# Kernel tuning notes

Measured on AMD Instinct MI355X. Metric: run time of the kernel, lower is better.

The kernel has to match this reference:

```python
import jax, jax.numpy as jnp
import numpy as np

B, T, C = 2, 2048, 1024
H, HS = 16, 64          # num_heads, head_size; H*HS == C
FF = 4 * C
EPS = 1e-5


def setup_inputs() -> dict:
    key = jax.random.key(0)
    ks = jax.random.split(key, 10)
    s = 0.02
    return {
        "x": jax.random.normal(ks[0], (B, T, C), dtype=jnp.float32),
        "Wq": jax.random.normal(ks[1], (H, C, HS), dtype=jnp.float32) * s,
        "Wk": jax.random.normal(ks[2], (H, C, HS), dtype=jnp.float32) * s,
        "Wv": jax.random.normal(ks[3], (H, C, HS), dtype=jnp.float32) * s,
        "p": jnp.ones((H,), dtype=jnp.float32),  # per-head learnable scale, init 1
        "Wproj": jax.random.normal(ks[4], (C, C), dtype=jnp.float32) * s,
        "W1": jax.random.normal(ks[5], (C, FF), dtype=jnp.float32) * s,
        "W2": jax.random.normal(ks[6], (FF, C), dtype=jnp.float32) * s,
        "ln1_w": jnp.ones((C,), dtype=jnp.float32),
        "ln1_b": jnp.zeros((C,), dtype=jnp.float32),
        "ln2_w": jnp.ones((C,), dtype=jnp.float32),
        "ln2_b": jnp.zeros((C,), dtype=jnp.float32),
    }


def _layernorm(x, w, b):
    mu = jnp.mean(x, axis=-1, keepdims=True)
    var = jnp.mean(jnp.square(x - mu), axis=-1, keepdims=True)
    return (x - mu) * jax.lax.rsqrt(var + EPS) * w + b


def reference(x, Wq, Wk, Wv, p, Wproj, W1, W2, ln1_w, ln1_b, ln2_w, ln2_b):
    # --- multi-head causal self-attention (dropout p=0 -> identity) ---
    h = _layernorm(x, ln1_w, ln1_b)
    q = jnp.einsum("btc,hcs->bhts", h, Wq)  # [B,H,T,HS]
    k = jnp.einsum("btc,hcs->bhts", h, Wk)
    v = jnp.einsum("btc,hcs->bhts", h, Wv)
    scale = p ** (-0.5)  # per-head scale, p init to 1
    wei = jnp.einsum("bhts,bhks->bhtk", q, k) * scale[None, :, None, None]
    causal = jnp.tril(jnp.ones((T, T), dtype=bool))
    wei = jnp.where(causal[None, None], wei, -jnp.inf)
    wei = jax.nn.softmax(wei, axis=-1)
    att = jnp.einsum("bhtk,bhks->bhts", wei, v)          # [B,H,T,HS]
    att = att.transpose(0, 2, 1, 3).reshape(B, T, C)     # concat heads
    sa = att @ Wproj
    x = x + sa
    # --- feed-forward (activation_id=0 -> ReLU) ---
    h2 = _layernorm(x, ln2_w, ln2_b)
    ff = jax.nn.relu(h2 @ W1) @ W2
    return x + ff
```

## Files before the change

### kernel.cpp

```cpp
#include <hip/hip_runtime.h>


typedef _Float16 f16;
typedef _Float16 f16x8 __attribute__((ext_vector_type(8)));
typedef _Float16 f16x4v __attribute__((ext_vector_type(4)));
typedef float f32x4 __attribute__((ext_vector_type(4)));

static constexpr int Tn = 2048;
static constexpr int Cn = 1024;
static constexpr int HSn = 64;

__device__ __forceinline__ void glds16(const f16* g, f16* l) {
    __builtin_amdgcn_global_load_lds((const __attribute__((address_space(1))) void*)g,
                                     (__attribute__((address_space(3))) void*)l,
                                     16, 0, 0);
}

#define VMCNT(N) asm volatile("s_waitcnt vmcnt(" #N ")" ::: "memory")
__device__ __forceinline__ void barrier_raw() {
    asm volatile("" ::: "memory");
    __builtin_amdgcn_s_barrier();
    asm volatile("" ::: "memory");
}

__device__ __forceinline__ unsigned cvt_pk_u32(float a, float b) {
    auto v = __builtin_amdgcn_cvt_pkrtz(a, b);
    union { __fp16 h2 __attribute__((ext_vector_type(2))); unsigned u; } c;
    c.h2 = v;
    return c.u;
}

__global__ __launch_bounds__(256) void ln_kernel(const float* __restrict__ x,
                                                 const float* __restrict__ w,
                                                 const float* __restrict__ b,
                                                 f16* __restrict__ out) {
    int row = blockIdx.x;
    const float* xr = x + (size_t)row * Cn;
    int tid = threadIdx.x, l = tid & 63, wv = tid >> 6;
    float4 v = *(const float4*)(xr + tid * 4);
    float s = v.x + v.y + v.z + v.w;
    float sq = v.x * v.x + v.y * v.y + v.z * v.z + v.w * v.w;
#pragma unroll
    for (int off = 32; off > 0; off >>= 1) {
        s += __shfl_down(s, off);
        sq += __shfl_down(sq, off);
    }
    __shared__ float red[8];
    if (l == 0) { red[wv] = s; red[wv + 4] = sq; }
    __syncthreads();
    float ts = red[0] + red[1] + red[2] + red[3];
    float tq = red[4] + red[5] + red[6] + red[7];
    float mean = ts * (1.0f / Cn);
    float var = tq * (1.0f / Cn) - mean * mean;
    float rstd = rsqrtf(var + 1e-5f);
    float4 wv4 = *(const float4*)(w + tid * 4);
    float4 bv4 = *(const float4*)(b + tid * 4);
    f16x4v o;
    o[0] = (f16)((v.x - mean) * rstd * wv4.x + bv4.x);
    o[1] = (f16)((v.y - mean) * rstd * wv4.y + bv4.y);
    o[2] = (f16)((v.z - mean) * rstd * wv4.z + bv4.z);
    o[3] = (f16)((v.w - mean) * rstd * wv4.w + bv4.w);
    *(f16x4v*)(out + (size_t)row * Cn + tid * 4) = o;
}

__global__ __launch_bounds__(256) void tr_cast_f32(const float* __restrict__ in, int irs,
                                                   f16* __restrict__ out, int ors) {
    __shared__ float tile[32][33];
    int r0 = blockIdx.x * 32, c0 = blockIdx.y * 32;
    int t = threadIdx.x;
    int rr = t >> 3, c4 = (t & 7) * 4;
    float4 v = *(const float4*)(in + (size_t)(r0 + rr) * irs + c0 + c4);
    tile[rr][c4] = v.x; tile[rr][c4 + 1] = v.y; tile[rr][c4 + 2] = v.z; tile[rr][c4 + 3] = v.w;
    __syncthreads();
    int cc = t >> 3, r4 = (t & 7) * 4;
    f16x4v o;
    o[0] = (f16)tile[r4][cc];
    o[1] = (f16)tile[r4 + 1][cc];
    o[2] = (f16)tile[r4 + 2][cc];
    o[3] = (f16)tile[r4 + 3][cc];
    *(f16x4v*)(out + (size_t)(c0 + cc) * ors + r0 + r4) = o;
}

__global__ __launch_bounds__(256) void tr_cast_qkv(const float* __restrict__ Wq,
                                                   const float* __restrict__ Wk,
                                                   const float* __restrict__ Wv,
                                                   f16* __restrict__ out) {
    int z = blockIdx.z;
    int qkv = z >> 4, h = z & 15;
    const float* in = (qkv == 0 ? Wq : qkv == 1 ? Wk : Wv) + (size_t)h * Cn * HSn;
    f16* o = out + (size_t)(qkv * Cn + h * HSn) * Cn;
    __shared__ float tile[32][33];
    int r0 = blockIdx.x * 32, c0 = blockIdx.y * 32;
    int t = threadIdx.x;
    int rr = t >> 3, c4 = (t & 7) * 4;
    float4 v = *(const float4*)(in + (size_t)(r0 + rr) * HSn + c0 + c4);
    tile[rr][c4] = v.x; tile[rr][c4 + 1] = v.y; tile[rr][c4 + 2] = v.z; tile[rr][c4 + 3] = v.w;
    __syncthreads();
    int cc = t >> 3, r4 = (t & 7) * 4;
    f16x4v ov;
    ov[0] = (f16)tile[r4][cc];
    ov[1] = (f16)tile[r4 + 1][cc];
    ov[2] = (f16)tile[r4 + 2][cc];
    ov[3] = (f16)tile[r4 + 3][cc];
    *(f16x4v*)(o + (size_t)(c0 + cc) * Cn + r0 + r4) = ov;
}

__global__ __launch_bounds__(256) void tr_vT(const f16* __restrict__ QKV, f16* __restrict__ vT) {
    int bh = blockIdx.z;
    int b = bh >> 4, h = bh & 15;
    const f16* in = QKV + (size_t)b * Tn * 3072 + 2048 + h * HSn;
    f16* out = vT + (size_t)bh * HSn * Tn;
    int r0 = blockIdx.x * 64;
    __shared__ __align__(16) f16 tile[64][72];
    int t = threadIdx.x;
#pragma unroll
    for (int i = 0; i < 2; i++) {
        int f = i * 256 + t;
        int rr = f >> 3, c8 = (f & 7) * 8;
        *(uint4*)(&tile[rr][c8]) = *(const uint4*)(in + (size_t)(r0 + rr) * 3072 + c8);
    }
    __syncthreads();
#pragma unroll
    for (int i = 0; i < 2; i++) {
        int f = i * 256 + t;
        int cc = f >> 3, r8 = (f & 7) * 8;
        union { f16 h[8]; uint4 v; } u;
#pragma unroll
        for (int j = 0; j < 8; j++) u.h[j] = tile[r8 + j][cc];
        *(uint4*)(out + (size_t)cc * Tn + r0 + r8) = u.v;
    }
}

template <int EPI>
__global__ __launch_bounds__(512, 2) void gemm8(const f16* __restrict__ A, const f16* __restrict__ Bt,
                                                f16* __restrict__ Cout, int M, int N, int K) {
    __shared__ __align__(16) f16 Abuf[4][8192];
    __shared__ __align__(16) f16 Bbuf[4][8192];
    int wg = blockIdx.x;
    int xcd = wg & 7, idx = wg >> 3;
    int bm = xcd * 2 + (idx & 1), bn = idx >> 1;
    int tid = threadIdx.x, l = tid & 63, w = tid >> 6;
    int wr = w >> 2, wc = w & 3;

    f32x4 acc[8][4];
#pragma unroll
    for (int m = 0; m < 8; m++)
#pragma unroll
        for (int n = 0; n < 4; n++) acc[m][n] = f32x4{0.f, 0.f, 0.f, 0.f};

    int l15 = l & 15;
    int lane_off = l15 * 32 + (((l >> 4) ^ ((l15 >> 1) & 3)) << 3);
    const f16* Afr = &Abuf[0][wr * 4096 + lane_off];
    const f16* Bfr = &Bbuf[0][(wc >> 1) * 4096 + (wc & 1) * 2048 + lane_off];

    int srow = w * 16 + (l >> 2);
    int schunk = (l & 3) ^ ((l >> 3) & 3);
    const f16* agp = A + (size_t)(bm * 256 + srow) * K + schunk * 8;
    const f16* bgp = Bt + (size_t)(bn * 256 + srow) * K + schunk * 8;
    const size_t rK = (size_t)128 * K;
    f16* dstA = &Abuf[0][w * 512];
    f16* dstB = &Bbuf[0][w * 512];

    auto stage = [&](int kt, int bf) {
        int k0 = kt * 32;
        glds16(agp + k0, dstA + bf * 8192);
        glds16(agp + rK + k0, dstA + bf * 8192 + 4096);
        glds16(bgp + k0, dstB + bf * 8192);
        glds16(bgp + rK + k0, dstB + bf * 8192 + 4096);
    };

    int NT = K >> 5;
    stage(0, 0);
    stage(1, 1);
    stage(2, 2);
    for (int t = 0; t < NT; ++t) {
        int cb = t & 3;
        if (t < NT - 2) VMCNT(8);
        else if (t == NT - 2) VMCNT(4);
        else VMCNT(0);
        barrier_raw();
        const f16* Ab = Afr + cb * 8192;
        const f16* Bb = Bfr + cb * 8192;
        f16x8 af[4], bf4[4];
#pragma unroll
        for (int m = 0; m < 4; m++) af[m] = *(const f16x8*)(Ab + m * 512);
#pragma unroll
        for (int n = 0; n < 4; n++) bf4[n] = *(const f16x8*)(Bb + n * 512);
        if (t + 3 < NT) stage(t + 3, (t + 3) & 3);
        __builtin_amdgcn_s_setprio(1);
#pragma unroll
        for (int m = 0; m < 4; m++)
#pragma unroll
            for (int n = 0; n < 4; n++)
                acc[m][n] = __builtin_amdgcn_mfma_f32_16x16x32_f16(af[m], bf4[n], acc[m][n], 0, 0, 0);
        __builtin_amdgcn_s_setprio(0);
        barrier_raw();
#pragma unroll
        for (int m = 0; m < 4; m++) af[m] = *(const f16x8*)(Ab + (m + 4) * 512);
        __builtin_amdgcn_s_setprio(1);
#pragma unroll
        for (int m = 0; m < 4; m++)
#pragma unroll
            for (int n = 0; n < 4; n++)
                acc[m + 4][n] = __builtin_amdgcn_mfma_f32_16x16x32_f16(af[m], bf4[n], acc[m + 4][n], 0, 0, 0);
        __builtin_amdgcn_s_setprio(0);
    }

    int row0 = bm * 256 + wr * 128 + (l >> 4) * 4;
    int col0 = bn * 256 + wc * 64 + (l & 15);
#pragma unroll
    for (int m = 0; m < 8; m++) {
#pragma unroll
        for (int n = 0; n < 4; n++) {
#pragma unroll
            for (int r = 0; r < 4; r++) {
                size_t idx = (size_t)(row0 + m * 16 + r) * N + (col0 + n * 16);
                float v = acc[m][n][r];
                if constexpr (EPI == 1) v = fmaxf(v, 0.f);
                Cout[idx] = (f16)v;
            }
        }
    }
}

__device__ __forceinline__ void l2_map(int& bm, int& bn) {
    int wg = blockIdx.y * 32 + blockIdx.x;
    int x = wg & 7, idx = wg >> 3;
    bm = x * 4 + (idx & 3);
    bn = idx >> 2;
}

template <int EPI>
__global__ __launch_bounds__(512) void gemm_ks(const f16* __restrict__ A, const f16* __restrict__ Bt,
                                               void* __restrict__ Cout, const float* __restrict__ resid,
                                               int M, int N, int K) {
    __shared__ __align__(16) char smem[131072];
    f16* As = (f16*)smem;
    f16* Bs = (f16*)(smem + 65536);
    int bm, bn;
    l2_map(bm, bn);
    int tid = threadIdx.x, l = tid & 63, w = tid >> 6;
    int grp = w >> 2, wl = w & 3;
    int wr = wl >> 1, wc = wl & 1;
    int Kh = K >> 1;
    int KT = Kh >> 5;

    f32x4 acc[4][4];
#pragma unroll
    for (int m = 0; m < 4; m++)
#pragma unroll
        for (int n = 0; n < 4; n++) acc[m][n] = f32x4{0.f, 0.f, 0.f, 0.f};

    int schunk = (l & 3) ^ ((l >> 3) & 3);
    const f16* agp = A + (size_t)(bm * 128 + wl * 16 + (l >> 2)) * K + grp * Kh + schunk * 8;
    const f16* bgp = Bt + (size_t)(bn * 128 + wl * 16 + (l >> 2)) * K + grp * Kh + schunk * 8;
    const size_t half = (size_t)64 * K;
    f16* Ab = As + grp * 16384;
    f16* Bb = Bs + grp * 16384;

    auto stage = [&](int kt, int bf) {
        size_t k0 = (size_t)kt * 32;
        glds16(agp + k0, Ab + bf * 4096 + wl * 512);
        glds16(agp + half + k0, Ab + bf * 4096 + 2048 + wl * 512);
        glds16(bgp + k0, Bb + bf * 4096 + wl * 512);
        glds16(bgp + half + k0, Bb + bf * 4096 + 2048 + wl * 512);
    };

    int l15 = l & 15;
    int rbase = (wr * 64 + l15) * 32 + (((l >> 4) ^ ((l15 >> 1) & 3)) << 3);
    int cbase = (wc * 64 + l15) * 32 + (((l >> 4) ^ ((l15 >> 1) & 3)) << 3);

    stage(0, 0);
    stage(1, 1);
    stage(2, 2);
    for (int kt = 0; kt < KT; ++kt) {
        int cb = kt & 3;
        if (kt < KT - 2) VMCNT(8);
        else if (kt == KT - 2) VMCNT(4);
        else VMCNT(0);
        barrier_raw();
        if (kt + 3 < KT) stage(kt + 3, (kt + 3) & 3);
        f16x8 af[4], bfr[4];
#pragma unroll
        for (int m = 0; m < 4; m++) af[m] = *(const f16x8*)(Ab + cb * 4096 + rbase + m * 512);
#pragma unroll
        for (int n = 0; n < 4; n++) bfr[n] = *(const f16x8*)(Bb + cb * 4096 + cbase + n * 512);
        __builtin_amdgcn_s_setprio(1);
#pragma unroll
        for (int m = 0; m < 4; m++)
#pragma unroll
            for (int n = 0; n < 4; n++)
                acc[m][n] = __builtin_amdgcn_mfma_f32_16x16x32_f16(af[m], bfr[n], acc[m][n], 0, 0, 0);
        __builtin_amdgcn_s_setprio(0);
    }
    __syncthreads();

    float* red = (float*)smem;
#pragma unroll
    for (int m = 0; m < 4; m++) {
        if (grp == 1) {
#pragma unroll
            for (int n = 0; n < 4; n++)
                *(f32x4*)(red + wl * 1280 + l * 20 + n * 4) = acc[m][n];
        }
        __syncthreads();
        if (grp == 0) {
#pragma unroll
            for (int n = 0; n < 4; n++)
                acc[m][n] += *(const f32x4*)(red + wl * 1280 + l * 20 + n * 4);
        }
        __syncthreads();
    }

    if (grp == 0) {
        int row0 = bm * 128 + wr * 64 + (l >> 4) * 4;
        int col0 = bn * 128 + wc * 64 + (l & 15);
#pragma unroll
        for (int m = 0; m < 4; m++) {
#pragma unroll
            for (int n = 0; n < 4; n++) {
#pragma unroll
                for (int r = 0; r < 4; r++) {
                    size_t idx = (size_t)(row0 + m * 16 + r) * N + (col0 + n * 16);
                    float v = acc[m][n][r];
                    if constexpr (EPI == 0) ((f16*)Cout)[idx] = (f16)v;
                    else if constexpr (EPI == 1) ((f16*)Cout)[idx] = (f16)fmaxf(v, 0.f);
                    else ((float*)Cout)[idx] = v + resid[idx];
                }
            }
        }
    }
}

__global__ __launch_bounds__(256) void attn_kernel(const f16* __restrict__ QKV,
                                                   const f16* __restrict__ vT,
                                                   const float* __restrict__ p,
                                                   f16* __restrict__ att) {
    int i = blockIdx.x;
    int bh = (i & 7) * 4 + ((i >> 3) & 3);
    int qt = 31 - (i >> 5);
    int b = bh >> 4, h = bh & 15;
    int tid = threadIdx.x, w = tid >> 6, l = tid & 63;
    float sc2 = rsqrtf(p[h]) * 1.44269504f;

    __shared__ __align__(16) f16 Ks[2][4096];
    __shared__ __align__(16) f16 Vs[2][4096];
    __shared__ __align__(16) f16 Ps[4][16 * 80];
    f16* Pw = &Ps[w][0];

    int srow0 = tid >> 3;
    int c0 = (tid & 7) ^ (srow0 & 7);
    const f16* Kg = QKV + (size_t)b * Tn * 3072 + 1024 + h * HSn;
    const f16* Vg = vT + (size_t)bh * HSn * Tn;
    const f16* Kg0 = Kg + (size_t)srow0 * 3072 + c0 * 8;
    const f16* Kg1 = Kg + (size_t)(srow0 + 32) * 3072 + c0 * 8;
    const f16* Vg0 = Vg + (size_t)srow0 * Tn + c0 * 8;
    const f16* Vg1 = Vg + (size_t)(srow0 + 32) * Tn + c0 * 8;
    int dl = w * 512 + l * 8;

    int foff[8];
#pragma unroll
    for (int n = 0; n < 4; n++)
#pragma unroll
        for (int ks = 0; ks < 2; ks++)
            foff[n * 2 + ks] = (n * 16 + (l & 15)) * 128 +
                               (((ks * 32 + (l >> 4) * 8) * 2) ^ ((l & 7) << 4));

    int qg = qt * 64 + w * 16 + (l & 15);
    int qo = qt * 64 + w * 16 + (l >> 4) * 4;
    const f16* qptr = QKV + (size_t)(b * Tn + qg) * 3072 + h * HSn + (l >> 4) * 8;
    f16x8 qf0 = *(const f16x8*)(qptr);
    f16x8 qf1 = *(const f16x8*)(qptr + 32);
    f16 sch = (f16)sc2;
#pragma unroll
    for (int j = 0; j < 8; j++) { qf0[j] *= sch; qf1[j] *= sch; }

    f32x4 o[4];
#pragma unroll
    for (int nf = 0; nf < 4; nf++) o[nf] = f32x4{0.f, 0.f, 0.f, 0.f};
    float m_r = -1e30f, l_r = 0.f;

    int nt = qt + 1;
    uint4 kr0 = *(const uint4*)(Kg0);
    uint4 kr1 = *(const uint4*)(Kg1);
    uint4 vr0 = *(const uint4*)(Vg0);
    uint4 vr1 = *(const uint4*)(Vg1);
    *(uint4*)(&Ks[0][dl]) = kr0;
    *(uint4*)(&Ks[0][2048 + dl]) = kr1;
    *(uint4*)(&Vs[0][dl]) = vr0;
    *(uint4*)(&Vs[0][2048 + dl]) = vr1;
    __syncthreads();
    for (int t = 0; t < nt; ++t) {
        int kv0 = t * 64;
        if (t + 1 < nt) {
            size_t ko = (size_t)(kv0 + 64) * 3072;
            kr0 = *(const uint4*)(Kg0 + ko);
            kr1 = *(const uint4*)(Kg1 + ko);
            vr0 = *(const uint4*)(Vg0 + kv0 + 64);
            vr1 = *(const uint4*)(Vg1 + kv0 + 64);
        }
        const char* Kb = (const char*)&Ks[t & 1][0];
        const char* Vb = (const char*)&Vs[t & 1][0];
        f32x4 s[4];
#pragma unroll
        for (int n = 0; n < 4; n++) s[n] = f32x4{0.f, 0.f, 0.f, 0.f};
        __builtin_amdgcn_s_setprio(1);
#pragma unroll
        for (int n = 0; n < 4; n++)
#pragma unroll
            for (int ks = 0; ks < 2; ks++) {
                f16x8 kf = *(const f16x8*)(Kb + foff[n * 2 + ks]);
                s[n] = __builtin_amdgcn_mfma_f32_16x16x32_f16(kf, ks == 0 ? qf0 : qf1, s[n], 0, 0, 0);
            }
        __builtin_amdgcn_s_setprio(0);
        if (t == qt) {
            int rel = qg - kv0;
#pragma unroll
            for (int n = 0; n < 4; n++)
#pragma unroll
                for (int r = 0; r < 4; r++) {
                    int kvr = n * 16 + (l >> 4) * 4 + r;
                    if (kvr > rel) s[n][r] = -1e30f;
                }
        }
        float tmax = -1e30f;
#pragma unroll
        for (int n = 0; n < 4; n++)
#pragma unroll
            for (int r = 0; r < 4; r++) tmax = fmaxf(tmax, s[n][r]);
        float lmul = 1.f;
        if (__any(tmax > m_r + 8.f)) {
            float rmax = fmaxf(tmax, __shfl_xor(tmax, 16));
            rmax = fmaxf(rmax, __shfl_xor(rmax, 32));
            float mnew = fmaxf(m_r, rmax);
            lmul = exp2f(m_r - mnew);
            m_r = mnew;
            float ar[4];
#pragma unroll
            for (int r = 0; r < 4; r++) ar[r] = __shfl(lmul, (l >> 4) * 4 + r);
#pragma unroll
            for (int nf = 0; nf < 4; nf++)
#pragma unroll
                for (int r = 0; r < 4; r++) o[nf][r] *= ar[r];
        }
        float rsum = 0.f;
#pragma unroll
        for (int n = 0; n < 4; n++) {
            float e0 = exp2f(s[n][0] - m_r), e1 = exp2f(s[n][1] - m_r);
            float e2 = exp2f(s[n][2] - m_r), e3 = exp2f(s[n][3] - m_r);
            rsum += (e0 + e1) + (e2 + e3);
            union { unsigned u[2]; f16x4v h4; } u;
            u.u[0] = cvt_pk_u32(e0, e1);
            u.u[1] = cvt_pk_u32(e2, e3);
            *(f16x4v*)(&Pw[(l & 15) * 80 + n * 16 + (l >> 4) * 4]) = u.h4;
        }
        l_r = l_r * lmul + rsum;
        f16x8 pa0 = *(const f16x8*)(&Pw[(l & 15) * 80 + (l >> 4) * 8]);
        f16x8 pa1 = *(const f16x8*)(&Pw[(l & 15) * 80 + 32 + (l >> 4) * 8]);
        __builtin_amdgcn_s_setprio(1);
#pragma unroll
        for (int nf = 0; nf < 4; nf++)
#pragma unroll
            for (int ks = 0; ks < 2; ks++) {
                f16x8 vf = *(const f16x8*)(Vb + foff[nf * 2 + ks]);
                o[nf] = __builtin_amdgcn_mfma_f32_16x16x32_f16(ks == 0 ? pa0 : pa1, vf, o[nf], 0, 0, 0);
            }
        __builtin_amdgcn_s_setprio(0);
        if (t + 1 < nt) {
            int nbf = (t + 1) & 1;
            *(uint4*)(&Ks[nbf][dl]) = kr0;
            *(uint4*)(&Ks[nbf][2048 + dl]) = kr1;
            *(uint4*)(&Vs[nbf][dl]) = vr0;
            *(uint4*)(&Vs[nbf][2048 + dl]) = vr1;
            __syncthreads();
        }
    }
    float lsum = l_r;
    lsum += __shfl_xor(lsum, 16);
    lsum += __shfl_xor(lsum, 32);
    float lro[4];
#pragma unroll
    for (int r = 0; r < 4; r++) lro[r] = __shfl(lsum, (l >> 4) * 4 + r);
#pragma unroll
    for (int nf = 0; nf < 4; nf++) {
#pragma unroll
        for (int r = 0; r < 4; r++) {
            float v = o[nf][r] / lro[r];
            att[(size_t)(b * Tn + qo + r) * Cn + h * HSn + nf * 16 + (l & 15)] = (f16)v;
        }
    }
}

extern "C" void kernel_launch(void* const* d_in, const int* in_sizes, int n_in,
                              void* d_out, int out_size, void* d_ws, size_t ws_size,
                              hipStream_t stream) {
    const float* x = (const float*)d_in[0];
    const float* Wq = (const float*)d_in[1];
    const float* Wk = (const float*)d_in[2];
    const float* Wv = (const float*)d_in[3];
    const float* p = (const float*)d_in[4];
    const float* Wproj = (const float*)d_in[5];
    const float* W1 = (const float*)d_in[6];
    const float* W2 = (const float*)d_in[7];
    const float* ln1w = (const float*)d_in[8];
    const float* ln1b = (const float*)d_in[9];
    const float* ln2w = (const float*)d_in[10];
    const float* ln2b = (const float*)d_in[11];

    char* ws = (char*)d_ws;
    const size_t MB = 1ull << 20;
    f16* Wqkv_t = (f16*)(ws + 0 * MB);
    f16* Wproj_t = (f16*)(ws + 6 * MB);
    f16* W1_t = (f16*)(ws + 8 * MB);
    f16* W2_t = (f16*)(ws + 16 * MB);
    float* x1 = (float*)(ws + 24 * MB);
    f16* QKV = (f16*)(ws + 40 * MB);
    f16* h1 = (f16*)(ws + 64 * MB);
    f16* vTb = (f16*)(ws + 64 * MB);
    f16* attb = (f16*)(ws + 72 * MB);
    f16* h2 = attb;
    f16* ffh = QKV;
    float* out = (float*)d_out;

    tr_cast_qkv<<<dim3(32, 2, 48), 256, 0, stream>>>(Wq, Wk, Wv, Wqkv_t);
    tr_cast_f32<<<dim3(32, 32), 256, 0, stream>>>(Wproj, 1024, Wproj_t, 1024);
    tr_cast_f32<<<dim3(32, 128), 256, 0, stream>>>(W1, 4096, W1_t, 1024);
    tr_cast_f32<<<dim3(128, 32), 256, 0, stream>>>(W2, 1024, W2_t, 4096);

    ln_kernel<<<4096, 256, 0, stream>>>(x, ln1w, ln1b, h1);
    gemm8<0><<<192, 512, 0, stream>>>(h1, Wqkv_t, QKV, 4096, 3072, 1024);
    tr_vT<<<dim3(32, 1, 32), 256, 0, stream>>>(QKV, vTb);
    attn_kernel<<<1024, 256, 0, stream>>>(QKV, vTb, p, attb);
    gemm_ks<2><<<dim3(32, 8), 512, 0, stream>>>(attb, Wproj_t, x1, x, 4096, 1024, 1024);
    ln_kernel<<<4096, 256, 0, stream>>>(x1, ln2w, ln2b, h2);
    gemm8<1><<<256, 512, 0, stream>>>(h2, W1_t, ffh, 4096, 4096, 1024);
    gemm_ks<2><<<dim3(32, 8), 512, 0, stream>>>(ffh, W2_t, out, x1, 4096, 1024, 4096);
}
```

Measured before the change: 217.8 us.

## Split-K the FF2 GEMM and widen attention blocks to 128 queries

Attention blocks grow to 512 threads covering two adjacent 64-row query tiles. Each K/V tile staged in shared memory is now reused by twice as many warps, and each thread loads one chunk instead of two. The second FFN GEMM becomes a 4-way split-K kernel with triple-buffered global-to-LDS loads, writing fp16 partials that a small epilogue kernel sums and adds to the residual. The intermediate x1 buffer goes away: the attention projection writes straight into the output. Rounding partial sums to fp16 adds precision loss, and the lower query-tile warps sit idle during the final KV tile.

```diff
diff --git a/kernel.cpp b/kernel.cpp
--- a/kernel.cpp
+++ b/kernel.cpp
@@ -223,6 +223,123 @@
     }
 }
 
+__global__ __launch_bounds__(512, 2) void gemm8s(const f16* __restrict__ A, const f16* __restrict__ Bt,
+                                                 f16* __restrict__ P0, f16* __restrict__ P1,
+                                                 f16* __restrict__ P2, f16* __restrict__ P3) {
+    constexpr int KF = 4096;
+    __shared__ __align__(16) f16 Abuf[4][8192];
+    __shared__ __align__(16) f16 Bbuf[4][8192];
+    int wg = blockIdx.x;
+    int xcd = wg & 7, idx = wg >> 3;
+    int bm = xcd * 2 + (idx & 1);
+    int r2 = idx >> 1;
+    int bn = r2 & 3, ks = r2 >> 2;
+    int k0g = ks * 1024;
+    int tid = threadIdx.x, l = tid & 63, w = tid >> 6;
+    int wr = w >> 2, wc = w & 3;
+
+    f32x4 acc[8][4];
+#pragma unroll
+    for (int m = 0; m < 8; m++)
+#pragma unroll
+        for (int n = 0; n < 4; n++) acc[m][n] = f32x4{0.f, 0.f, 0.f, 0.f};
+
+    int l15 = l & 15;
+    int lane_off = l15 * 32 + (((l >> 4) ^ ((l15 >> 1) & 3)) << 3);
+    const f16* Afr = &Abuf[0][wr * 4096 + lane_off];
+    const f16* Bfr = &Bbuf[0][(wc >> 1) * 4096 + (wc & 1) * 2048 + lane_off];
+
+    int srow = w * 16 + (l >> 2);
+    int schunk = (l & 3) ^ ((l >> 3) & 3);
+    const f16* agp = A + (size_t)(bm * 256 + srow) * KF + k0g + schunk * 8;
+    const f16* bgp = Bt + (size_t)(bn * 256 + srow) * KF + k0g + schunk * 8;
+    const size_t rK = (size_t)128 * KF;
+    f16* dstA = &Abuf[0][w * 512];
+    f16* dstB = &Bbuf[0][w * 512];
+
+    auto stage = [&](int kt, int bf) {
+        int k0 = kt * 32;
+        glds16(agp + k0, dstA + bf * 8192);
+        glds16(agp + rK + k0, dstA + bf * 8192 + 4096);
+        glds16(bgp + k0, dstB + bf * 8192);
+        glds16(bgp + rK + k0, dstB + bf * 8192 + 4096);
+    };
+
+    constexpr int NT = 32;
+    stage(0, 0);
+    stage(1, 1);
+    stage(2, 2);
+    for (int t = 0; t < NT; ++t) {
+        int cb = t & 3;
+        if (t < NT - 2) VMCNT(8);
+        else if (t == NT - 2) VMCNT(4);
+        else VMCNT(0);
+        barrier_raw();
+        const f16* Ab = Afr + cb * 8192;
+        const f16* Bb = Bfr + cb * 8192;
+        f16x8 af[4], bf4[4];
+#pragma unroll
+        for (int m = 0; m < 4; m++) af[m] = *(const f16x8*)(Ab + m * 512);
+#pragma unroll
+        for (int n = 0; n < 4; n++) bf4[n] = *(const f16x8*)(Bb + n * 512);
+        if (t + 3 < NT) stage(t + 3, (t + 3) & 3);
+        __builtin_amdgcn_s_setprio(1);
+#pragma unroll
+        for (int m = 0; m < 4; m++)
+#pragma unroll
+            for (int n = 0; n < 4; n++)
+                acc[m][n] = __builtin_amdgcn_mfma_f32_16x16x32_f16(af[m], bf4[n], acc[m][n], 0, 0, 0);
+        __builtin_amdgcn_s_setprio(0);
+        barrier_raw();
+#pragma unroll
+        for (int m = 0; m < 4; m++) af[m] = *(const f16x8*)(Ab + (m + 4) * 512);
+        __builtin_amdgcn_s_setprio(1);
+#pragma unroll
+        for (int m = 0; m < 4; m++)
+#pragma unroll
+            for (int n = 0; n < 4; n++)
+                acc[m + 4][n] = __builtin_amdgcn_mfma_f32_16x16x32_f16(af[m], bf4[n], acc[m + 4][n], 0, 0, 0);
+        __builtin_amdgcn_s_setprio(0);
+    }
+
+    f16* P = (ks == 0) ? P0 : (ks == 1) ? P1 : (ks == 2) ? P2 : P3;
+    int row0 = bm * 256 + wr * 128 + (l >> 4) * 4;
+    int col0 = bn * 256 + wc * 64 + (l & 15);
+#pragma unroll
+    for (int m = 0; m < 8; m++) {
+#pragma unroll
+        for (int n = 0; n < 4; n++) {
+#pragma unroll
+            for (int r = 0; r < 4; r++) {
+                size_t idx = (size_t)(row0 + m * 16 + r) * 1024 + (col0 + n * 16);
+                P[idx] = (f16)acc[m][n][r];
+            }
+        }
+    }
+}
+
+__global__ __launch_bounds__(256) void ff2_epi(const f16* __restrict__ p0q,
+                                               const f16* __restrict__ p1q,
+                                               const f16* __restrict__ p2q,
+                                               const f16* __restrict__ p3q,
+                                               float* __restrict__ out) {
+    size_t base = ((size_t)blockIdx.x * 256 + threadIdx.x) * 8;
+    f16x8 p0 = *(const f16x8*)(p0q + base);
+    f16x8 p1 = *(const f16x8*)(p1q + base);
+    f16x8 p2 = *(const f16x8*)(p2q + base);
+    f16x8 p3 = *(const f16x8*)(p3q + base);
+    float4 r0 = *(const float4*)(out + base);
+    float4 r1 = *(const float4*)(out + base + 4);
+    float o[8];
+#pragma unroll
+    for (int j = 0; j < 8; j++)
+        o[j] = ((float)p0[j] + (float)p1[j]) + ((float)p2[j] + (float)p3[j]);
+    float4 w0 = {o[0] + r0.x, o[1] + r0.y, o[2] + r0.z, o[3] + r0.w};
+    float4 w1 = {o[4] + r1.x, o[5] + r1.y, o[6] + r1.z, o[7] + r1.w};
+    *(float4*)(out + base) = w0;
+    *(float4*)(out + base + 4) = w1;
+}
+
 __device__ __forceinline__ void l2_map(int& bm, int& bn) {
     int wg = blockIdx.y * 32 + blockIdx.x;
     int x = wg & 7, idx = wg >> 3;
@@ -332,31 +449,30 @@
     }
 }
 
-__global__ __launch_bounds__(256) void attn_kernel(const f16* __restrict__ QKV,
+__global__ __launch_bounds__(512) void attn_kernel(const f16* __restrict__ QKV,
                                                    const f16* __restrict__ vT,
                                                    const float* __restrict__ p,
                                                    f16* __restrict__ att) {
-    int i = blockIdx.x;
-    int bh = (i & 7) * 4 + ((i >> 3) & 3);
-    int qt = 31 - (i >> 5);
+    int idx = blockIdx.x;
+    int bh = (idx & 7) * 4 + ((idx >> 3) & 3);
+    int ip = 15 - (idx >> 5);
     int b = bh >> 4, h = bh & 15;
     int tid = threadIdx.x, w = tid >> 6, l = tid & 63;
+    int half = w >> 2, wl = w & 3;
     float sc2 = rsqrtf(p[h]) * 1.44269504f;
 
     __shared__ __align__(16) f16 Ks[2][4096];
     __shared__ __align__(16) f16 Vs[2][4096];
-    __shared__ __align__(16) f16 Ps[4][16 * 80];
+    __shared__ __align__(16) f16 Ps[8][16 * 80];
     f16* Pw = &Ps[w][0];
 
-    int srow0 = tid >> 3;
-    int c0 = (tid & 7) ^ (srow0 & 7);
+    int srow = tid >> 3;
+    int c0 = (tid & 7) ^ (srow & 7);
     const f16* Kg = QKV + (size_t)b * Tn * 3072 + 1024 + h * HSn;
     const f16* Vg = vT + (size_t)bh * HSn * Tn;
-    const f16* Kg0 = Kg + (size_t)srow0 * 3072 + c0 * 8;
-    const f16* Kg1 = Kg + (size_t)(srow0 + 32) * 3072 + c0 * 8;
-    const f16* Vg0 = Vg + (size_t)srow0 * Tn + c0 * 8;
-    const f16* Vg1 = Vg + (size_t)(srow0 + 32) * Tn + c0 * 8;
-    int dl = w * 512 + l * 8;
+    const f16* Kg0 = Kg + (size_t)srow * 3072 + c0 * 8;
+    const f16* Vg0 = Vg + (size_t)srow * Tn + c0 * 8;
+    int dl = tid * 8;
 
     int foff[8];
 #pragma unroll
@@ -366,8 +482,9 @@
             foff[n * 2 + ks] = (n * 16 + (l & 15)) * 128 +
                                (((ks * 32 + (l >> 4) * 8) * 2) ^ ((l & 7) << 4));
 
-    int qg = qt * 64 + w * 16 + (l & 15);
-    int qo = qt * 64 + w * 16 + (l >> 4) * 4;
+    int qtw = 2 * ip + half;
+    int qg = ip * 128 + half * 64 + wl * 16 + (l & 15);
+    int qo = ip * 128 + half * 64 + wl * 16 + (l >> 4) * 4;
     const f16* qptr = QKV + (size_t)(b * Tn + qg) * 3072 + h * HSn + (l >> 4) * 8;
     f16x8 qf0 = *(const f16x8*)(qptr);
     f16x8 qf1 = *(const f16x8*)(qptr + 32);
@@ -380,98 +497,91 @@
     for (int nf = 0; nf < 4; nf++) o[nf] = f32x4{0.f, 0.f, 0.f, 0.f};
     float m_r = -1e30f, l_r = 0.f;
 
-    int nt = qt + 1;
-    uint4 kr0 = *(const uint4*)(Kg0);
-    uint4 kr1 = *(const uint4*)(Kg1);
-    uint4 vr0 = *(const uint4*)(Vg0);
-    uint4 vr1 = *(const uint4*)(Vg1);
-    *(uint4*)(&Ks[0][dl]) = kr0;
-    *(uint4*)(&Ks[0][2048 + dl]) = kr1;
-    *(uint4*)(&Vs[0][dl]) = vr0;
-    *(uint4*)(&Vs[0][2048 + dl]) = vr1;
+    int nt = 2 * ip + 2;
+    uint4 kr = *(const uint4*)(Kg0);
+    uint4 vr = *(const uint4*)(Vg0);
+    *(uint4*)(&Ks[0][dl]) = kr;
+    *(uint4*)(&Vs[0][dl]) = vr;
     __syncthreads();
     for (int t = 0; t < nt; ++t) {
         int kv0 = t * 64;
         if (t + 1 < nt) {
-            size_t ko = (size_t)(kv0 + 64) * 3072;
-            kr0 = *(const uint4*)(Kg0 + ko);
-            kr1 = *(const uint4*)(Kg1 + ko);
-            vr0 = *(const uint4*)(Vg0 + kv0 + 64);
-            vr1 = *(const uint4*)(Vg1 + kv0 + 64);
-        }
-        const char* Kb = (const char*)&Ks[t & 1][0];
-        const char* Vb = (const char*)&Vs[t & 1][0];
-        f32x4 s[4];
-#pragma unroll
-        for (int n = 0; n < 4; n++) s[n] = f32x4{0.f, 0.f, 0.f, 0.f};
-        __builtin_amdgcn_s_setprio(1);
-#pragma unroll
-        for (int n = 0; n < 4; n++)
-#pragma unroll
-            for (int ks = 0; ks < 2; ks++) {
-                f16x8 kf = *(const f16x8*)(Kb + foff[n * 2 + ks]);
-                s[n] = __builtin_amdgcn_mfma_f32_16x16x32_f16(kf, ks == 0 ? qf0 : qf1, s[n], 0, 0, 0);
+            kr = *(const uint4*)(Kg0 + (size_t)(kv0 + 64) * 3072);
+            vr = *(const uint4*)(Vg0 + kv0 + 64);
+        }
+        if (t <= qtw) {
+            const char* Kb = (const char*)&Ks[t & 1][0];
+            const char* Vb = (const char*)&Vs[t & 1][0];
+            f32x4 s[4];
+#pragma unroll
+            for (int n = 0; n < 4; n++) s[n] = f32x4{0.f, 0.f, 0.f, 0.f};
+            __builtin_amdgcn_s_setprio(1);
+#pragma unroll
+            for (int n = 0; n < 4; n++)
+#pragma unroll
+                for (int ks = 0; ks < 2; ks++) {
+                    f16x8 kf = *(const f16x8*)(Kb + foff[n * 2 + ks]);
+                    s[n] = __builtin_amdgcn_mfma_f32_16x16x32_f16(kf, ks == 0 ? qf0 : qf1, s[n], 0, 0, 0);
+                }
+            __builtin_amdgcn_s_setprio(0);
+            if (t == qtw) {
+                int rel = qg - kv0;
+#pragma unroll
+                for (int n = 0; n < 4; n++)
+#pragma unroll
+                    for (int r = 0; r < 4; r++) {
+                        int kvr = n * 16 + (l >> 4) * 4 + r;
+                        if (kvr > rel) s[n][r] = -1e30f;
+                    }
             }
-        __builtin_amdgcn_s_setprio(0);
-        if (t == qt) {
-            int rel = qg - kv0;
-#pragma unroll
-            for (int n = 0; n < 4; n++)
-#pragma unroll
-                for (int r = 0; r < 4; r++) {
-                    int kvr = n * 16 + (l >> 4) * 4 + r;
-                    if (kvr > rel) s[n][r] = -1e30f;
+            float tmax = -1e30f;
+#pragma unroll
+            for (int n = 0; n < 4; n++)
+#pragma unroll
+                for (int r = 0; r < 4; r++) tmax = fmaxf(tmax, s[n][r]);
+            float lmul = 1.f;
+            if (__any(tmax > m_r + 8.f)) {
+                float rmax = fmaxf(tmax, __shfl_xor(tmax, 16));
+                rmax = fmaxf(rmax, __shfl_xor(rmax, 32));
+                float mnew = fmaxf(m_r, rmax);
+                lmul = exp2f(m_r - mnew);
+                m_r = mnew;
+                float ar[4];
+#pragma unroll
+                for (int r = 0; r < 4; r++) ar[r] = __shfl(lmul, (l >> 4) * 4 + r);
+#pragma unroll
+                for (int nf = 0; nf < 4; nf++)
+#pragma unroll
+                    for (int r = 0; r < 4; r++) o[nf][r] *= ar[r];
+            }
+            float rsum = 0.f;
+#pragma unroll
+            for (int n = 0; n < 4; n++) {
+                float e0 = exp2f(s[n][0] - m_r), e1 = exp2f(s[n][1] - m_r);
+                float e2 = exp2f(s[n][2] - m_r), e3 = exp2f(s[n][3] - m_r);
+                rsum += (e0 + e1) + (e2 + e3);
+                union { unsigned u[2]; f16x4v h4; } u;
+                u.u[0] = cvt_pk_u32(e0, e1);
+                u.u[1] = cvt_pk_u32(e2, e3);
+                *(f16x4v*)(&Pw[(l & 15) * 80 + n * 16 + (l >> 4) * 4]) = u.h4;
+            }
+            l_r = l_r * lmul + rsum;
+            f16x8 pa0 = *(const f16x8*)(&Pw[(l & 15) * 80 + (l >> 4) * 8]);
+            f16x8 pa1 = *(const f16x8*)(&Pw[(l & 15) * 80 + 32 + (l >> 4) * 8]);
+            __builtin_amdgcn_s_setprio(1);
+#pragma unroll
+            for (int nf = 0; nf < 4; nf++)
+#pragma unroll
+                for (int ks = 0; ks < 2; ks++) {
+                    f16x8 vf = *(const f16x8*)(Vb + foff[nf * 2 + ks]);
+                    o[nf] = __builtin_amdgcn_mfma_f32_16x16x32_f16(ks == 0 ? pa0 : pa1, vf, o[nf], 0, 0, 0);
                 }
-        }
-        float tmax = -1e30f;
-#pragma unroll
-        for (int n = 0; n < 4; n++)
-#pragma unroll
-            for (int r = 0; r < 4; r++) tmax = fmaxf(tmax, s[n][r]);
-        float lmul = 1.f;
-        if (__any(tmax > m_r + 8.f)) {
-            float rmax = fmaxf(tmax, __shfl_xor(tmax, 16));
-            rmax = fmaxf(rmax, __shfl_xor(rmax, 32));
-            float mnew = fmaxf(m_r, rmax);
-            lmul = exp2f(m_r - mnew);
-            m_r = mnew;
-            float ar[4];
-#pragma unroll
-            for (int r = 0; r < 4; r++) ar[r] = __shfl(lmul, (l >> 4) * 4 + r);
-#pragma unroll
-            for (int nf = 0; nf < 4; nf++)
-#pragma unroll
-                for (int r = 0; r < 4; r++) o[nf][r] *= ar[r];
-        }
-        float rsum = 0.f;
-#pragma unroll
-        for (int n = 0; n < 4; n++) {
-            float e0 = exp2f(s[n][0] - m_r), e1 = exp2f(s[n][1] - m_r);
-            float e2 = exp2f(s[n][2] - m_r), e3 = exp2f(s[n][3] - m_r);
-            rsum += (e0 + e1) + (e2 + e3);
-            union { unsigned u[2]; f16x4v h4; } u;
-            u.u[0] = cvt_pk_u32(e0, e1);
-            u.u[1] = cvt_pk_u32(e2, e3);
-            *(f16x4v*)(&Pw[(l & 15) * 80 + n * 16 + (l >> 4) * 4]) = u.h4;
-        }
-        l_r = l_r * lmul + rsum;
-        f16x8 pa0 = *(const f16x8*)(&Pw[(l & 15) * 80 + (l >> 4) * 8]);
-        f16x8 pa1 = *(const f16x8*)(&Pw[(l & 15) * 80 + 32 + (l >> 4) * 8]);
-        __builtin_amdgcn_s_setprio(1);
-#pragma unroll
-        for (int nf = 0; nf < 4; nf++)
-#pragma unroll
-            for (int ks = 0; ks < 2; ks++) {
-                f16x8 vf = *(const f16x8*)(Vb + foff[nf * 2 + ks]);
-                o[nf] = __builtin_amdgcn_mfma_f32_16x16x32_f16(ks == 0 ? pa0 : pa1, vf, o[nf], 0, 0, 0);
-            }
-        __builtin_amdgcn_s_setprio(0);
+            __builtin_amdgcn_s_setprio(0);
+        }
         if (t + 1 < nt) {
             int nbf = (t + 1) & 1;
-            *(uint4*)(&Ks[nbf][dl]) = kr0;
-            *(uint4*)(&Ks[nbf][2048 + dl]) = kr1;
-            *(uint4*)(&Vs[nbf][dl]) = vr0;
-            *(uint4*)(&Vs[nbf][2048 + dl]) = vr1;
+            *(uint4*)(&Ks[nbf][dl]) = kr;
+            *(uint4*)(&Vs[nbf][dl]) = vr;
             __syncthreads();
         }
     }
@@ -513,13 +623,16 @@
     f16* Wproj_t = (f16*)(ws + 6 * MB);
     f16* W1_t = (f16*)(ws + 8 * MB);
     f16* W2_t = (f16*)(ws + 16 * MB);
-    float* x1 = (float*)(ws + 24 * MB);
     f16* QKV = (f16*)(ws + 40 * MB);
     f16* h1 = (f16*)(ws + 64 * MB);
     f16* vTb = (f16*)(ws + 64 * MB);
     f16* attb = (f16*)(ws + 72 * MB);
     f16* h2 = attb;
     f16* ffh = QKV;
+    f16* p0 = (f16*)(ws + 0 * MB);
+    f16* p1 = (f16*)(ws + 8 * MB);
+    f16* p2 = (f16*)(ws + 24 * MB);
+    f16* p3 = (f16*)(ws + 32 * MB);
     float* out = (float*)d_out;
 
     tr_cast_qkv<<<dim3(32, 2, 48), 256, 0, stream>>>(Wq, Wk, Wv, Wqkv_t);
@@ -530,9 +643,10 @@
     ln_kernel<<<4096, 256, 0, stream>>>(x, ln1w, ln1b, h1);
     gemm8<0><<<192, 512, 0, stream>>>(h1, Wqkv_t, QKV, 4096, 3072, 1024);
     tr_vT<<<dim3(32, 1, 32), 256, 0, stream>>>(QKV, vTb);
-    attn_kernel<<<1024, 256, 0, stream>>>(QKV, vTb, p, attb);
-    gemm_ks<2><<<dim3(32, 8), 512, 0, stream>>>(attb, Wproj_t, x1, x, 4096, 1024, 1024);
-    ln_kernel<<<4096, 256, 0, stream>>>(x1, ln2w, ln2b, h2);
+    attn_kernel<<<512, 512, 0, stream>>>(QKV, vTb, p, attb);
+    gemm_ks<2><<<dim3(32, 8), 512, 0, stream>>>(attb, Wproj_t, out, x, 4096, 1024, 1024);
+    ln_kernel<<<4096, 256, 0, stream>>>(out, ln2w, ln2b, h2);
     gemm8<1><<<256, 512, 0, stream>>>(h2, W1_t, ffh, 4096, 4096, 1024);
-    gemm_ks<2><<<dim3(32, 8), 512, 0, stream>>>(ffh, W2_t, out, x1, 4096, 1024, 4096);
-}
+    gemm8s<<<256, 512, 0, stream>>>(ffh, W2_t, p0, p1, p2, p3);
+    ff2_epi<<<2048, 256, 0, stream>>>(p0, p1, p2, p3, out);
+}
```

After: 228.1 us. 4.7% more time.
